# Optimization experiments

Measured on AMD Instinct MI355X. Metric: run time of the kernel, lower is better.

The kernel has to match this reference:

```python
import jax, jax.numpy as jnp
import numpy as np
from jax import lax

DIM = 768
D_STATE = 16
D_CONV = 4
EXPAND = 2
DT_RANK = 32
D_INNER = EXPAND * DIM
BATCH = 2
SEQ = 1024


def setup_inputs() -> dict:
    key = jax.random.key(0)
    ks = jax.random.split(key, 10)
    x = jax.random.normal(ks[0], (BATCH, SEQ, DIM), dtype=jnp.float32)
    W_in = jax.random.normal(ks[1], (2 * D_INNER, DIM), dtype=jnp.float32) * (DIM ** -0.5)
    W_conv = jax.random.normal(ks[2], (D_INNER, 1, D_CONV), dtype=jnp.float32) * (D_CONV ** -0.5)
    b_conv = jax.random.normal(ks[3], (D_INNER,), dtype=jnp.float32) * 0.02
    W_x = jax.random.normal(ks[4], (DT_RANK + 2 * D_STATE, D_INNER), dtype=jnp.float32) * (D_INNER ** -0.5)
    dt_init_std = DT_RANK ** -0.5
    W_dt = jax.random.uniform(ks[5], (D_INNER, DT_RANK), dtype=jnp.float32, minval=-dt_init_std, maxval=dt_init_std)
    # dt bias: inverse-softplus of dt sampled loguniform in [dt_min, dt_max]
    dt = jnp.exp(jax.random.uniform(ks[6], (D_INNER,), dtype=jnp.float32) * (np.log(0.1) - np.log(0.001)) + np.log(0.001))
    dt = jnp.clip(dt, 1e-4, None)
    b_dt = dt + jnp.log(-jnp.expm1(-dt))
    A_log = jnp.log(jnp.broadcast_to(jnp.arange(1, D_STATE + 1, dtype=jnp.float32), (D_INNER, D_STATE)))
    D = jnp.ones((D_INNER,), dtype=jnp.float32)
    W_out = jax.random.normal(ks[7], (DIM, D_INNER), dtype=jnp.float32) * (D_INNER ** -0.5)
    return {"x": x, "W_in": W_in, "W_conv": W_conv, "b_conv": b_conv, "W_x": W_x,
            "W_dt": W_dt, "b_dt": b_dt, "A_log": A_log, "D": D, "W_out": W_out}


def _silu(v):
    return v * jax.nn.sigmoid(v)


def reference(x, W_in, W_conv, b_conv, W_x, W_dt, b_dt, A_log, D, W_out):
    b, l, d = x.shape
    residual = x
    # in_proj and split into x / gate z
    xz = jnp.einsum('bld,ed->ble', x, W_in)           # (b,l,2*d_inner)
    xc, z = jnp.split(xz, 2, axis=-1)
    # depthwise causal conv1d (left pad d_conv-1, then original slices to seq_len)
    xc = lax.conv_general_dilated(
        xc.transpose(0, 2, 1), W_conv, window_strides=(1,),
        padding=[(D_CONV - 1, 0)], feature_group_count=D_INNER)
    xc = (xc + b_conv[None, :, None]).transpose(0, 2, 1)  # (b,l,d_inner)
    xc = _silu(xc)
    # x_proj -> dt, B, C
    x_dbl = jnp.einsum('bld,ed->ble', xc, W_x)
    dt_lr = x_dbl[..., :DT_RANK]
    B = x_dbl[..., DT_RANK:DT_RANK + D_STATE]
    C = x_dbl[..., DT_RANK + D_STATE:]
    # NOTE: original adds dt_proj bias twice (once inside Linear, once explicitly)
    dt = jax.nn.softplus(jnp.einsum('blr,dr->bld', dt_lr, W_dt) + b_dt + b_dt)
    A = -jnp.exp(A_log)                                # (d_inner, d_state)
    deltaA = jnp.exp(dt[..., None] * A[None, None])    # (b,l,d_inner,d_state)
    dBu = dt[..., None] * B[:, :, None, :] * xc[..., None]
    # sequential selective scan: h_t = deltaA_t * h_{t-1} + dBu_t
    def step(h, inp):
        a, bu = inp
        h = a * h + bu
        return h, h
    h0 = jnp.zeros((b, D_INNER, D_STATE), dtype=xc.dtype)
    _, hs = lax.scan(step, h0, (deltaA.transpose(1, 0, 2, 3), dBu.transpose(1, 0, 2, 3)))
    hs = hs.transpose(1, 0, 2, 3)                      # (b,l,d_inner,d_state)
    y = jnp.sum(hs * C[:, :, None, :], axis=3) + xc * D[None, None, :]
    y = y * _silu(z)
    out = jnp.einsum('bld,ed->ble', y, W_out)
    # dropout is identity in eval mode
    return out + residual
```

## Files before the change

### kernel.cpp

```cpp
#include <hip/hip_runtime.h>
#include <stdint.h>

#define DIM 768
#define D_STATE 16
#define D_CONV 4
#define DT_RANK 32
#define D_INNER 1536
#define BATCH 2
#define SEQ 1024
#define BL (BATCH * SEQ)
#define E2 (2 * D_INNER)
#define NCHUNK 64
#define TC (SEQ / NCHUNK)
#define XKS 8
#define XKC (D_INNER / XKS)

typedef __attribute__((ext_vector_type(8))) __bf16 bf16x8;
typedef __attribute__((ext_vector_type(4))) float f32x4;
typedef __attribute__((ext_vector_type(8))) unsigned short u16x8;

__device__ __forceinline__ float silu_f(float v) {
    return v / (1.0f + __expf(-v));
}
__device__ __forceinline__ float softplus_f(float v) {
    return fmaxf(v, 0.0f) + __logf(1.0f + __expf(-fabsf(v)));
}
__device__ __forceinline__ unsigned short f2bf(float f) {
    uint32_t u = __float_as_uint(f);
    u += 0x7FFFu + ((u >> 16) & 1u);
    return (unsigned short)(u >> 16);
}
__device__ __forceinline__ float bf2f(unsigned short u) {
    return __uint_as_float((uint32_t)u << 16);
}
__device__ __forceinline__ void gload_lds16(const void* g, void* l) {
    __builtin_amdgcn_global_load_lds(
        (const __attribute__((address_space(1))) unsigned int*)(uintptr_t)g,
        (__attribute__((address_space(3))) unsigned int*)(uint32_t)(uintptr_t)l,
        16, 0, 0);
}

__global__ __launch_bounds__(256) void cvt5_kernel(
    const float* __restrict__ s0, unsigned short* __restrict__ d0, int n0,
    const float* __restrict__ s1, unsigned short* __restrict__ d1, int n1,
    const float* __restrict__ s2, unsigned short* __restrict__ d2, int n2,
    const float* __restrict__ s3, unsigned short* __restrict__ d3, int n3,
    const float* __restrict__ s4, unsigned short* __restrict__ d4, int n4)
{
    int i = blockIdx.x * 256 + threadIdx.x;
    const float* s; unsigned short* d;
    if (i < n0)                          { s = s0; d = d0; }
    else if ((i -= n0) < n1)             { s = s1; d = d1; }
    else if ((i -= n1) < n2)             { s = s2; d = d2; }
    else if ((i -= n2) < n3)             { s = s3; d = d3; }
    else { i -= n3; if (i >= n4) return;   s = s4; d = d4; }
    const f32x4 a = ((const f32x4*)s)[2 * i];
    const f32x4 b = ((const f32x4*)s)[2 * i + 1];
    u16x8 o;
#pragma unroll
    for (int j = 0; j < 4; ++j) { o[j] = f2bf(a[j]); o[4 + j] = f2bf(b[j]); }
    ((u16x8*)d)[i] = o;
}

template <int BM, int BN, int EPI>
__global__ __launch_bounds__(256) void gemm_bf16(
    const unsigned short* __restrict__ A, const unsigned short* __restrict__ B,
    void* __restrict__ C, int ldc,
    const float* __restrict__ X, int ldx, int K)
{
    constexpr int NROW = BM + BN;
    constexpr int RW = NROW / 4;
    constexpr int NC = RW / 16;
    constexpr int FM = BM / 32;
    constexpr int FN = BN / 32;
    __shared__ __align__(16) unsigned short S[2][NROW * 32];
    const int tid = threadIdx.x;
    const int wid = tid >> 6;
    const int lane = tid & 63;
    const int wr = wid >> 1, wc = wid & 1;
    const int bm = blockIdx.y * BM, bn = blockIdx.x * BN;

    const int lrow = lane >> 2;
    const int scol = (lane & 3) * 8;
    const unsigned short* gsrc[NC];
#pragma unroll
    for (int c = 0; c < NC; ++c) {
        const int rowbase = wid * RW + c * 16;
        const int grow = rowbase + lrow;
        gsrc[c] = (rowbase < BM)
            ? A + (size_t)(bm + grow) * K + scol
            : B + (size_t)(bn + grow - BM) * K + scol;
    }

    const int fr = lane & 15;
    const int fq = lane >> 4;
    f32x4 acc[FM][FN] = {};

    auto STAGE = [&](int nb, int k0) {
#pragma unroll
        for (int c = 0; c < NC; ++c)
            gload_lds16(gsrc[c] + k0, &S[nb][(wid * RW + c * 16) * 32]);
    };
    auto COMPUTE = [&](int cb) {
        bf16x8 af[FM], bfr[FN];
#pragma unroll
        for (int m = 0; m < FM; ++m)
            af[m] = *(const bf16x8*)&S[cb][(wr * (BM / 2) + m * 16 + fr) * 32 + fq * 8];
#pragma unroll
        for (int n = 0; n < FN; ++n)
            bfr[n] = *(const bf16x8*)&S[cb][(BM + wc * (BN / 2) + n * 16 + fr) * 32 + fq * 8];
#pragma unroll
        for (int m = 0; m < FM; ++m)
#pragma unroll
            for (int n = 0; n < FN; ++n)
                acc[m][n] = __builtin_amdgcn_mfma_f32_16x16x32_bf16(
                    af[m], bfr[n], acc[m][n], 0, 0, 0);
    };

    STAGE(0, 0);
    asm volatile("s_waitcnt vmcnt(0)" ::: "memory");
    __builtin_amdgcn_s_barrier();
    int cur = 0;
    for (int k0 = 32; k0 < K; k0 += 32) {
        STAGE(cur ^ 1, k0);
        COMPUTE(cur);
        asm volatile("s_waitcnt vmcnt(0)" ::: "memory");
        __builtin_amdgcn_s_barrier();
        cur ^= 1;
    }
    COMPUTE(cur);

#pragma unroll
    for (int m = 0; m < FM; ++m) {
#pragma unroll
        for (int n = 0; n < FN; ++n) {
            const int col = bn + wc * (BN / 2) + n * 16 + fr;
#pragma unroll
            for (int r = 0; r < 4; ++r) {
                const int row = bm + wr * (BM / 2) + m * 16 + fq * 4 + r;
                float o = acc[m][n][r];
                if (EPI == 0) {
                    ((float*)C)[(size_t)row * ldc + col] = o;
                } else if (EPI == 1) {
                    o = softplus_f(o + 2.0f * X[col]);
                    ((unsigned short*)C)[(size_t)row * ldc + col] = f2bf(o);
                } else if (EPI == 2) {
                    o += X[(size_t)row * ldx + col];
                    ((float*)C)[(size_t)row * ldc + col] = o;
                } else {
                    ((unsigned short*)C)[(size_t)row * ldc + col] = f2bf(o);
                }
            }
        }
    }
}

__global__ __launch_bounds__(256) void xdbl_gemm(
    const unsigned short* __restrict__ xcsb,
    const unsigned short* __restrict__ W_x_b,
    float* __restrict__ part)
{
    constexpr int BM = 128, NROW = BM + 64, RW = NROW / 4, NC = RW / 16;
    __shared__ __align__(16) unsigned short S[2][NROW * 32];
    const int tid = threadIdx.x;
    const int wid = tid >> 6, lane = tid & 63;
    const int wr = wid >> 1, wc = wid & 1;
    const int bm = blockIdx.y * BM;
    const int kb = blockIdx.x * XKC;
    const int lrow = lane >> 2, scol = (lane & 3) * 8;
    const unsigned short* gsrc[NC];
#pragma unroll
    for (int c = 0; c < NC; ++c) {
        const int rowbase = wid * RW + c * 16;
        const int grow = rowbase + lrow;
        gsrc[c] = (rowbase < BM)
            ? xcsb + (size_t)(bm + grow) * D_INNER + kb + scol
            : W_x_b + (size_t)(grow - BM) * D_INNER + kb + scol;
    }
    const int fr = lane & 15, fq = lane >> 4;
    f32x4 acc[4][2] = {};
    auto STAGE = [&](int nb, int k0) {
#pragma unroll
        for (int c = 0; c < NC; ++c)
            gload_lds16(gsrc[c] + k0, &S[nb][(wid * RW + c * 16) * 32]);
    };
    auto COMPUTE = [&](int cb) {
        bf16x8 af[4], bfr[2];
#pragma unroll
        for (int m = 0; m < 4; ++m)
            af[m] = *(const bf16x8*)&S[cb][(wr * 64 + m * 16 + fr) * 32 + fq * 8];
#pragma unroll
        for (int n = 0; n < 2; ++n)
            bfr[n] = *(const bf16x8*)&S[cb][(BM + wc * 32 + n * 16 + fr) * 32 + fq * 8];
#pragma unroll
        for (int m = 0; m < 4; ++m)
#pragma unroll
            for (int n = 0; n < 2; ++n)
                acc[m][n] = __builtin_amdgcn_mfma_f32_16x16x32_bf16(
                    af[m], bfr[n], acc[m][n], 0, 0, 0);
    };
    STAGE(0, 0);
    asm volatile("s_waitcnt vmcnt(0)" ::: "memory");
    __builtin_amdgcn_s_barrier();
    int cur = 0;
    for (int k0 = 32; k0 < XKC; k0 += 32) {
        STAGE(cur ^ 1, k0);
        COMPUTE(cur);
        asm volatile("s_waitcnt vmcnt(0)" ::: "memory");
        __builtin_amdgcn_s_barrier();
        cur ^= 1;
    }
    COMPUTE(cur);
    float* P = part + (size_t)blockIdx.x * BL * 64;
#pragma unroll
    for (int m = 0; m < 4; ++m)
#pragma unroll
        for (int n = 0; n < 2; ++n) {
            const int col = wc * 32 + n * 16 + fr;
#pragma unroll
            for (int r = 0; r < 4; ++r) {
                const int row = bm + wr * 64 + m * 16 + fq * 4 + r;
                P[(size_t)row * 64 + col] = acc[m][n][r];
            }
        }
}

__global__ __launch_bounds__(256) void xdbl_reduce(
    const float* __restrict__ part, float* __restrict__ xdbl,
    unsigned short* __restrict__ dtlrb)
{
    const int i = blockIdx.x * 256 + threadIdx.x;
    if (i >= BL * 64) return;
    float s = 0.0f;
#pragma unroll
    for (int ks = 0; ks < XKS; ++ks) s += part[(size_t)ks * (BL * 64) + i];
    xdbl[i] = s;
    const int col = i & 63, row = i >> 6;
    if (col < 32) dtlrb[row * 32 + col] = f2bf(s);
}

__global__ __launch_bounds__(256) void conv_silu_kernel(
    const unsigned short* __restrict__ xzb, const float* __restrict__ Wc,
    const float* __restrict__ bc, unsigned short* __restrict__ xcsb)
{
    const int i8 = blockIdx.x * 256 + threadIdx.x;
    if (i8 >= BL * D_INNER / 8) return;
    const int dg = i8 % (D_INNER / 8);
    const int bl = i8 / (D_INNER / 8);
    const int l = bl % SEQ;
    const int d0 = dg * 8;
    const size_t rowb = (size_t)bl * E2 + d0;

    const u16x8 x0 = *(const u16x8*)&xzb[rowb];
    u16x8 x1 = {}, x2 = {}, x3 = {};
    if (l >= 1) x1 = *(const u16x8*)&xzb[rowb - E2];
    if (l >= 2) x2 = *(const u16x8*)&xzb[rowb - 2 * E2];
    if (l >= 3) x3 = *(const u16x8*)&xzb[rowb - 3 * E2];
    const f32x4 b0 = *(const f32x4*)&bc[d0];
    const f32x4 b1 = *(const f32x4*)&bc[d0 + 4];

    u16x8 o;
#pragma unroll
    for (int j = 0; j < 8; ++j) {
        const f32x4 w = *(const f32x4*)&Wc[(size_t)(d0 + j) * 4];
        float acc = (j < 4 ? b0[j] : b1[j - 4]);
        acc += w[3] * bf2f(x0[j]);
        acc += w[2] * bf2f(x1[j]);
        acc += w[1] * bf2f(x2[j]);
        acc += w[0] * bf2f(x3[j]);
        o[j] = f2bf(silu_f(acc));
    }
    *(u16x8*)&xcsb[(size_t)bl * D_INNER + d0] = o;
}

__global__ __launch_bounds__(256) void scan_p1(
    const unsigned short* __restrict__ dtgb, const unsigned short* __restrict__ xcsb,
    const float* __restrict__ xdbl, const float* __restrict__ A_log,
    unsigned short* __restrict__ Hc, float* __restrict__ sdt_arr)
{
    __shared__ unsigned short dt_s[TC][256];
    __shared__ unsigned short xc_s[TC][256];
    __shared__ float Bsh[TC][16];
    const int tid = threadIdx.x;
    const int d0 = blockIdx.x * 256;
    const int d = d0 + tid;
    const int c = blockIdx.y;
    const int b = blockIdx.z;
    const int r0 = b * SEQ + c * TC;

#pragma unroll
    for (int k = 0; k < TC * 32 / 256; ++k) {
        const int u = k * 256 + tid;
        const int t = u >> 5, c8 = (u & 31) * 8;
        *(u16x8*)&dt_s[t][c8] = *(const u16x8*)&dtgb[(size_t)(r0 + t) * D_INNER + d0 + c8];
        *(u16x8*)&xc_s[t][c8] = *(const u16x8*)&xcsb[(size_t)(r0 + t) * D_INNER + d0 + c8];
    }
    {
        const int t = tid >> 4, j = tid & 15;
        Bsh[t][j] = xdbl[(size_t)(r0 + t) * 64 + 32 + j];
    }
    float a[16];
#pragma unroll
    for (int q = 0; q < 4; ++q) {
        const f32x4 al = *(const f32x4*)&A_log[(size_t)d * 16 + q * 4];
#pragma unroll
        for (int j = 0; j < 4; ++j) a[q * 4 + j] = -__expf(al[j]);
    }
    __syncthreads();

    float h[16];
#pragma unroll
    for (int s = 0; s < 16; ++s) h[s] = 0.0f;
    float sdt = 0.0f;
#pragma unroll
    for (int t = 0; t < TC; ++t) {
        const float dt = bf2f(dt_s[t][tid]);
        const float xc = bf2f(xc_s[t][tid]);
        sdt += dt;
        const float u = dt * xc;
        const f32x4 B0 = *(const f32x4*)&Bsh[t][0];
        const f32x4 B1 = *(const f32x4*)&Bsh[t][4];
        const f32x4 B2 = *(const f32x4*)&Bsh[t][8];
        const f32x4 B3 = *(const f32x4*)&Bsh[t][12];
#pragma unroll
        for (int s = 0; s < 16; ++s) {
            const float Bv = (s < 4 ? B0[s] : s < 8 ? B1[s - 4] : s < 12 ? B2[s - 8] : B3[s - 12]);
            h[s] = __expf(dt * a[s]) * h[s] + u * Bv;
        }
    }
    const size_t o = (((size_t)b * NCHUNK + c) * D_INNER + d) * 16;
    u16x8 h0, h1;
#pragma unroll
    for (int j = 0; j < 8; ++j) { h0[j] = f2bf(h[j]); h1[j] = f2bf(h[8 + j]); }
    *(u16x8*)&Hc[o] = h0;
    *(u16x8*)&Hc[o + 8] = h1;
    sdt_arr[((size_t)b * NCHUNK + c) * D_INNER + d] = sdt;
}

__global__ __launch_bounds__(256) void scan_p2(
    unsigned short* __restrict__ Hc, const float* __restrict__ sdt_arr,
    const float* __restrict__ A_log)
{
    const int idx = blockIdx.x * 256 + threadIdx.x;
    if (idx >= BATCH * D_INNER * 16) return;
    const int b = idx / (D_INNER * 16);
    const int ds = idx % (D_INNER * 16);
    const int d = ds >> 4;
    const float a = -__expf(A_log[ds]);
    const size_t hstep = (size_t)D_INNER * 16;
    const size_t sstep = (size_t)D_INNER;
    size_t oh = (size_t)b * NCHUNK * hstep + ds;
    size_t os = (size_t)b * NCHUNK * sstep + d;

    float hc0 = bf2f(Hc[oh]);             float sd0 = sdt_arr[os];
    float hc1 = bf2f(Hc[oh + hstep]);     float sd1 = sdt_arr[os + sstep];
    float hc2 = bf2f(Hc[oh + 2 * hstep]); float sd2 = sdt_arr[os + 2 * sstep];
    float hc3 = bf2f(Hc[oh + 3 * hstep]); float sd3 = sdt_arr[os + 3 * sstep];
    float h = 0.0f;

#pragma unroll
    for (int c = 0; c < NCHUNK; c += 4) {
        {
            const float E = __expf(sd0 * a);
            Hc[oh] = f2bf(h);
            h = E * h + hc0;
            if (c + 4 < NCHUNK) { hc0 = bf2f(Hc[oh + 4 * hstep]); sd0 = sdt_arr[os + 4 * sstep]; }
            oh += hstep; os += sstep;
        }
        {
            const float E = __expf(sd1 * a);
            Hc[oh] = f2bf(h);
            h = E * h + hc1;
            if (c + 5 < NCHUNK) { hc1 = bf2f(Hc[oh + 4 * hstep]); sd1 = sdt_arr[os + 4 * sstep]; }
            oh += hstep; os += sstep;
        }
        {
            const float E = __expf(sd2 * a);
            Hc[oh] = f2bf(h);
            h = E * h + hc2;
            if (c + 6 < NCHUNK) { hc2 = bf2f(Hc[oh + 4 * hstep]); sd2 = sdt_arr[os + 4 * sstep]; }
            oh += hstep; os += sstep;
        }
        {
            const float E = __expf(sd3 * a);
            Hc[oh] = f2bf(h);
            h = E * h + hc3;
            if (c + 7 < NCHUNK) { hc3 = bf2f(Hc[oh + 4 * hstep]); sd3 = sdt_arr[os + 4 * sstep]; }
            oh += hstep; os += sstep;
        }
    }
}

__global__ __launch_bounds__(256) void scan_p3(
    const unsigned short* __restrict__ dtgb, const unsigned short* __restrict__ xcsb,
    const float* __restrict__ xdbl, const float* __restrict__ A_log,
    const float* __restrict__ Dp, const unsigned short* __restrict__ Hinit,
    const unsigned short* __restrict__ xzb, unsigned short* __restrict__ ymb)
{
    __shared__ unsigned short dt_s[TC][256];
    __shared__ unsigned short xc_s[TC][256];
    __shared__ unsigned short z_s[TC][256];
    __shared__ float BCsh[TC][32];
    const int tid = threadIdx.x;
    const int d0 = blockIdx.x * 256;
    const int d = d0 + tid;
    const int c = blockIdx.y;
    const int b = blockIdx.z;
    const int r0 = b * SEQ + c * TC;

#pragma unroll
    for (int k = 0; k < TC * 32 / 256; ++k) {
        const int u = k * 256 + tid;
        const int t = u >> 5, c8 = (u & 31) * 8;
        *(u16x8*)&dt_s[t][c8] = *(const u16x8*)&dtgb[(size_t)(r0 + t) * D_INNER + d0 + c8];
        *(u16x8*)&xc_s[t][c8] = *(const u16x8*)&xcsb[(size_t)(r0 + t) * D_INNER + d0 + c8];
        *(u16x8*)&z_s[t][c8]  = *(const u16x8*)&xzb[(size_t)(r0 + t) * E2 + D_INNER + d0 + c8];
    }
    for (int i = tid; i < TC * 32; i += 256) {
        const int t = i >> 5, j = i & 31;
        BCsh[t][j] = xdbl[(size_t)(r0 + t) * 64 + 32 + j];
    }
    float a[16];
#pragma unroll
    for (int q = 0; q < 4; ++q) {
        const f32x4 al = *(const f32x4*)&A_log[(size_t)d * 16 + q * 4];
#pragma unroll
        for (int j = 0; j < 4; ++j) a[q * 4 + j] = -__expf(al[j]);
    }
    const float Dd = Dp[d];
    float h[16];
    {
        const size_t o = (((size_t)b * NCHUNK + c) * D_INNER + d) * 16;
        const u16x8 h0 = *(const u16x8*)&Hinit[o];
        const u16x8 h1 = *(const u16x8*)&Hinit[o + 8];
#pragma unroll
        for (int j = 0; j < 8; ++j) { h[j] = bf2f(h0[j]); h[8 + j] = bf2f(h1[j]); }
    }
    __syncthreads();

    const size_t base = (size_t)r0 * D_INNER + d;
#pragma unroll
    for (int t = 0; t < TC; ++t) {
        const float dt = bf2f(dt_s[t][tid]);
        const float xc = bf2f(xc_s[t][tid]);
        const float z  = bf2f(z_s[t][tid]);
        const float u = dt * xc;
        const f32x4 B0 = *(const f32x4*)&BCsh[t][0];
        const f32x4 B1 = *(const f32x4*)&BCsh[t][4];
        const f32x4 B2 = *(const f32x4*)&BCsh[t][8];
        const f32x4 B3 = *(const f32x4*)&BCsh[t][12];
        const f32x4 C0 = *(const f32x4*)&BCsh[t][16];
        const f32x4 C1 = *(const f32x4*)&BCsh[t][20];
        const f32x4 C2 = *(const f32x4*)&BCsh[t][24];
        const f32x4 C3 = *(const f32x4*)&BCsh[t][28];
        float y = 0.0f;
#pragma unroll
        for (int s = 0; s < 16; ++s) {
            const float Bv = (s < 4 ? B0[s] : s < 8 ? B1[s - 4] : s < 12 ? B2[s - 8] : B3[s - 12]);
            const float Cv = (s < 4 ? C0[s] : s < 8 ? C1[s - 4] : s < 12 ? C2[s - 8] : C3[s - 12]);
            h[s] = __expf(dt * a[s]) * h[s] + u * Bv;
            y += h[s] * Cv;
        }
        y += xc * Dd;
        ymb[base + (size_t)t * D_INNER] = f2bf(y * silu_f(z));
    }
}

extern "C" void kernel_launch(void* const* d_in, const int* in_sizes, int n_in,
                              void* d_out, int out_size, void* d_ws, size_t ws_size,
                              hipStream_t stream) {
    const float* x      = (const float*)d_in[0];
    const float* W_in   = (const float*)d_in[1];
    const float* W_conv = (const float*)d_in[2];
    const float* b_conv = (const float*)d_in[3];
    const float* W_x    = (const float*)d_in[4];
    const float* W_dt   = (const float*)d_in[5];
    const float* b_dt   = (const float*)d_in[6];
    const float* A_log  = (const float*)d_in[7];
    const float* Dp     = (const float*)d_in[8];
    const float* W_out  = (const float*)d_in[9];
    float* out = (float*)d_out;

    char* p = (char*)d_ws;
    auto alloc = [&](size_t bytes) { char* r = p; p += (bytes + 255) & ~(size_t)255; return r; };
    unsigned short* xzb     = (unsigned short*)alloc((size_t)BL * E2 * 2);
    unsigned short* xcsb    = (unsigned short*)alloc((size_t)BL * D_INNER * 2);
    unsigned short* dtgb    = (unsigned short*)alloc((size_t)BL * D_INNER * 2);
    unsigned short* ymb     = (unsigned short*)alloc((size_t)BL * D_INNER * 2);
    unsigned short* dtlrb   = (unsigned short*)alloc((size_t)BL * 32 * 2);
    unsigned short* xb      = (unsigned short*)alloc((size_t)BL * DIM * 2);
    unsigned short* W_in_b  = (unsigned short*)alloc((size_t)E2 * DIM * 2);
    unsigned short* W_out_b = (unsigned short*)alloc((size_t)DIM * D_INNER * 2);
    unsigned short* W_x_b   = (unsigned short*)alloc((size_t)64 * D_INNER * 2);
    unsigned short* W_dt_b  = (unsigned short*)alloc((size_t)D_INNER * DT_RANK * 2);
    float* xdbl             = (float*)alloc((size_t)BL * 64 * 4);
    float* part             = (float*)alloc((size_t)XKS * BL * 64 * 4);
    unsigned short* Hc      = (unsigned short*)alloc((size_t)BATCH * NCHUNK * D_INNER * 16 * 2);
    float* sdt              = (float*)alloc((size_t)BATCH * NCHUNK * D_INNER * 4);

    cvt5_kernel<<<(294912 + 196608 + 147456 + 12288 + 6144) / 256, 256, 0, stream>>>(
        W_in, W_in_b, E2 * DIM / 8,
        x, xb, BL * DIM / 8,
        W_out, W_out_b, DIM * D_INNER / 8,
        W_x, W_x_b, 64 * D_INNER / 8,
        W_dt, W_dt_b, D_INNER * DT_RANK / 8);
    gemm_bf16<128, 128, 3><<<dim3(E2 / 128, BL / 128), 256, 0, stream>>>(
        xb, W_in_b, xzb, E2, nullptr, 0, DIM);
    conv_silu_kernel<<<(BL * D_INNER / 8) / 256, 256, 0, stream>>>(
        xzb, W_conv, b_conv, xcsb);
    xdbl_gemm<<<dim3(XKS, BL / 128), 256, 0, stream>>>(xcsb, W_x_b, part);
    xdbl_reduce<<<(BL * 64) / 256, 256, 0, stream>>>(part, xdbl, dtlrb);
    gemm_bf16<64, 64, 1><<<dim3(D_INNER / 64, BL / 64), 256, 0, stream>>>(
        dtlrb, W_dt_b, dtgb, D_INNER, b_dt, 0, DT_RANK);
    scan_p1<<<dim3(D_INNER / 256, NCHUNK, BATCH), 256, 0, stream>>>(
        dtgb, xcsb, xdbl, A_log, Hc, sdt);
    scan_p2<<<(BATCH * D_INNER * 16) / 256, 256, 0, stream>>>(Hc, sdt, A_log);
    scan_p3<<<dim3(D_INNER / 256, NCHUNK, BATCH), 256, 0, stream>>>(
        dtgb, xcsb, xdbl, A_log, Dp, Hc, xzb, ymb);
    gemm_bf16<64, 64, 2><<<dim3(DIM / 64, BL / 64), 256, 0, stream>>>(
        ymb, W_out_b, out, DIM, x, DIM, D_INNER);
}
```

Baseline: 108.3 us.

## Fuse dt projection into xdbl reduce and swizzle GEMM block order across XCDs

The dt_proj GEMM and its softplus epilogue are folded into the xdbl reduction kernel. Each block now computes four rows of dt in fp32 directly from W_dt, which removes a kernel launch, the dtlrb intermediate and the W_dt bf16 conversion. The remaining bf16 GEMMs use a 1D grid with a block-index swizzle spread across the 8 XCDs, aiming at better L2 locality. The trade-off is that every reduce block reloads the full W_dt, 196KB per block across 512 blocks, which the cache has to absorb.

After: 122.5 us. 13.1% more time.

```diff
diff --git a/kernel.cpp b/kernel.cpp
--- a/kernel.cpp
+++ b/kernel.cpp
@@ -40,20 +40,18 @@
         16, 0, 0);
 }
 
-__global__ __launch_bounds__(256) void cvt5_kernel(
+__global__ __launch_bounds__(256) void cvt4_kernel(
     const float* __restrict__ s0, unsigned short* __restrict__ d0, int n0,
     const float* __restrict__ s1, unsigned short* __restrict__ d1, int n1,
     const float* __restrict__ s2, unsigned short* __restrict__ d2, int n2,
-    const float* __restrict__ s3, unsigned short* __restrict__ d3, int n3,
-    const float* __restrict__ s4, unsigned short* __restrict__ d4, int n4)
+    const float* __restrict__ s3, unsigned short* __restrict__ d3, int n3)
 {
     int i = blockIdx.x * 256 + threadIdx.x;
     const float* s; unsigned short* d;
     if (i < n0)                          { s = s0; d = d0; }
     else if ((i -= n0) < n1)             { s = s1; d = d1; }
     else if ((i -= n1) < n2)             { s = s2; d = d2; }
-    else if ((i -= n2) < n3)             { s = s3; d = d3; }
-    else { i -= n3; if (i >= n4) return;   s = s4; d = d4; }
+    else { i -= n2; if (i >= n3) return;   s = s3; d = d3; }
     const f32x4 a = ((const f32x4*)s)[2 * i];
     const f32x4 b = ((const f32x4*)s)[2 * i + 1];
     u16x8 o;
@@ -66,7 +64,7 @@
 __global__ __launch_bounds__(256) void gemm_bf16(
     const unsigned short* __restrict__ A, const unsigned short* __restrict__ B,
     void* __restrict__ C, int ldc,
-    const float* __restrict__ X, int ldx, int K)
+    const float* __restrict__ X, int ldx, int K, int nbx)
 {
     constexpr int NROW = BM + BN;
     constexpr int RW = NROW / 4;
@@ -78,7 +76,11 @@
     const int wid = tid >> 6;
     const int lane = tid & 63;
     const int wr = wid >> 1, wc = wid & 1;
-    const int bm = blockIdx.y * BM, bn = blockIdx.x * BN;
+
+    const int nwg = gridDim.x;
+    const int bid = blockIdx.x;
+    const int swz = (bid & 7) * (nwg >> 3) + (bid >> 3);
+    const int bm = (swz / nbx) * BM, bn = (swz % nbx) * BN;
 
     const int lrow = lane >> 2;
     const int scol = (lane & 3) * 8;
@@ -141,9 +143,6 @@
                 float o = acc[m][n][r];
                 if (EPI == 0) {
                     ((float*)C)[(size_t)row * ldc + col] = o;
-                } else if (EPI == 1) {
-                    o = softplus_f(o + 2.0f * X[col]);
-                    ((unsigned short*)C)[(size_t)row * ldc + col] = f2bf(o);
                 } else if (EPI == 2) {
                     o += X[(size_t)row * ldx + col];
                     ((float*)C)[(size_t)row * ldc + col] = o;
@@ -225,18 +224,49 @@
         }
 }
 
-__global__ __launch_bounds__(256) void xdbl_reduce(
+__global__ __launch_bounds__(256) void xdbl_reduce_dt(
     const float* __restrict__ part, float* __restrict__ xdbl,
-    unsigned short* __restrict__ dtlrb)
-{
-    const int i = blockIdx.x * 256 + threadIdx.x;
-    if (i >= BL * 64) return;
+    const float* __restrict__ W_dt, const float* __restrict__ b_dt,
+    unsigned short* __restrict__ dtgb)
+{
+    __shared__ float sums[4][32];
+    const int tid = threadIdx.x;
+    const int i = blockIdx.x * 256 + tid;
     float s = 0.0f;
 #pragma unroll
     for (int ks = 0; ks < XKS; ++ks) s += part[(size_t)ks * (BL * 64) + i];
     xdbl[i] = s;
-    const int col = i & 63, row = i >> 6;
-    if (col < 32) dtlrb[row * 32 + col] = f2bf(s);
+    const int col = i & 63;
+    const int rowl = tid >> 6;
+    if (col < 32) sums[rowl][col] = s;
+    __syncthreads();
+
+    const int row0 = blockIdx.x * 4;
+#pragma unroll
+    for (int k = 0; k < 6; ++k) {
+        const int d = k * 256 + tid;
+        const float b2 = 2.0f * b_dt[d];
+        f32x4 w[8];
+#pragma unroll
+        for (int q = 0; q < 8; ++q) w[q] = *(const f32x4*)&W_dt[(size_t)d * 32 + q * 4];
+        float acc0 = b2, acc1 = b2, acc2 = b2, acc3 = b2;
+#pragma unroll
+        for (int q = 0; q < 8; ++q) {
+#pragma unroll
+            for (int j = 0; j < 4; ++j) {
+                const float wv = w[q][j];
+                const int jj = q * 4 + j;
+                acc0 += wv * sums[0][jj];
+                acc1 += wv * sums[1][jj];
+                acc2 += wv * sums[2][jj];
+                acc3 += wv * sums[3][jj];
+            }
+        }
+        dtgb[(size_t)(row0 + 0) * D_INNER + d] = f2bf(softplus_f(acc0));
+        dtgb[(size_t)(row0 + 1) * D_INNER + d] = f2bf(softplus_f(acc1));
+        dtgb[(size_t)(row0 + 2) * D_INNER + d] = f2bf(softplus_f(acc2));
+        dtgb[(size_t)(row0 + 3) * D_INNER + d] = f2bf(softplus_f(acc3));
+    }
 }
 
 __global__ __launch_bounds__(256) void conv_silu_kernel(
@@ -487,36 +517,32 @@
     unsigned short* xcsb    = (unsigned short*)alloc((size_t)BL * D_INNER * 2);
     unsigned short* dtgb    = (unsigned short*)alloc((size_t)BL * D_INNER * 2);
     unsigned short* ymb     = (unsigned short*)alloc((size_t)BL * D_INNER * 2);
-    unsigned short* dtlrb   = (unsigned short*)alloc((size_t)BL * 32 * 2);
     unsigned short* xb      = (unsigned short*)alloc((size_t)BL * DIM * 2);
     unsigned short* W_in_b  = (unsigned short*)alloc((size_t)E2 * DIM * 2);
     unsigned short* W_out_b = (unsigned short*)alloc((size_t)DIM * D_INNER * 2);
     unsigned short* W_x_b   = (unsigned short*)alloc((size_t)64 * D_INNER * 2);
-    unsigned short* W_dt_b  = (unsigned short*)alloc((size_t)D_INNER * DT_RANK * 2);
     float* xdbl             = (float*)alloc((size_t)BL * 64 * 4);
     float* part             = (float*)alloc((size_t)XKS * BL * 64 * 4);
     unsigned short* Hc      = (unsigned short*)alloc((size_t)BATCH * NCHUNK * D_INNER * 16 * 2);
     float* sdt              = (float*)alloc((size_t)BATCH * NCHUNK * D_INNER * 4);
 
-    cvt5_kernel<<<(294912 + 196608 + 147456 + 12288 + 6144) / 256, 256, 0, stream>>>(
+    cvt4_kernel<<<(294912 + 196608 + 147456 + 12288) / 256, 256, 0, stream>>>(
         W_in, W_in_b, E2 * DIM / 8,
         x, xb, BL * DIM / 8,
         W_out, W_out_b, DIM * D_INNER / 8,
-        W_x, W_x_b, 64 * D_INNER / 8,
-        W_dt, W_dt_b, D_INNER * DT_RANK / 8);
-    gemm_bf16<128, 128, 3><<<dim3(E2 / 128, BL / 128), 256, 0, stream>>>(
-        xb, W_in_b, xzb, E2, nullptr, 0, DIM);
+        W_x, W_x_b, 64 * D_INNER / 8);
+    gemm_bf16<128, 128, 3><<<(E2 / 128) * (BL / 128), 256, 0, stream>>>(
+        xb, W_in_b, xzb, E2, nullptr, 0, DIM, E2 / 128);
     conv_silu_kernel<<<(BL * D_INNER / 8) / 256, 256, 0, stream>>>(
         xzb, W_conv, b_conv, xcsb);
     xdbl_gemm<<<dim3(XKS, BL / 128), 256, 0, stream>>>(xcsb, W_x_b, part);
-    xdbl_reduce<<<(BL * 64) / 256, 256, 0, stream>>>(part, xdbl, dtlrb);
-    gemm_bf16<64, 64, 1><<<dim3(D_INNER / 64, BL / 64), 256, 0, stream>>>(
-        dtlrb, W_dt_b, dtgb, D_INNER, b_dt, 0, DT_RANK);
+    xdbl_reduce_dt<<<(BL * 64) / 256, 256, 0, stream>>>(
+        part, xdbl, W_dt, b_dt, dtgb);
     scan_p1<<<dim3(D_INNER / 256, NCHUNK, BATCH), 256, 0, stream>>>(
         dtgb, xcsb, xdbl, A_log, Hc, sdt);
     scan_p2<<<(BATCH * D_INNER * 16) / 256, 256, 0, stream>>>(Hc, sdt, A_log);
     scan_p3<<<dim3(D_INNER / 256, NCHUNK, BATCH), 256, 0, stream>>>(
         dtgb, xcsb, xdbl, A_log, Dp, Hc, xzb, ymb);
-    gemm_bf16<64, 64, 2><<<dim3(DIM / 64, BL / 64), 256, 0, stream>>>(
-        ymb, W_out_b, out, DIM, x, DIM, D_INNER);
-}
+    gemm_bf16<64, 64, 2><<<(DIM / 64) * (BL / 64), 256, 0, stream>>>(
+        ymb, W_out_b, out, DIM, x, DIM, D_INNER, DIM / 64);
+}
```
